# Kernel optimization log

Hardware: AMD Instinct MI355X
Metric: run time of the kernel (lower is better)

Reference implementation:

```python
import jax, jax.numpy as jnp
import numpy as np

B, T, D = 2, 4096, 1024
HQ, HKV, HD = 16, 4, 64   # 16 query heads, 4 KV heads (kv_groups=4), head_dim=64
WIN = 256                 # sliding window radius (left == right == 256)


def setup_inputs() -> dict:
    key = jax.random.key(0)
    ks = jax.random.split(key, 9)
    s = 0.02  # small init scale for stable softmax logits
    return {
        "x": jax.random.normal(ks[0], (B, T, D), jnp.float32),
        "wq": jax.random.normal(ks[1], (D, HQ * HD), jnp.float32) * s,
        "bq": jnp.zeros((HQ * HD,), jnp.float32),
        "wk": jax.random.normal(ks[2], (D, HKV * HD), jnp.float32) * s,
        "bk": jnp.zeros((HKV * HD,), jnp.float32),
        "wv": jax.random.normal(ks[3], (D, HKV * HD), jnp.float32) * s,
        "bv": jnp.zeros((HKV * HD,), jnp.float32),
        "wo": jax.random.normal(ks[4], (HQ * HD, D), jnp.float32) * s,
        "bo": jnp.zeros((D,), jnp.float32),
    }


def _banded_gqa(q, k, v, left, right):
    """Sliding-window GQA attention: query i attends keys in [i-left, i+right].
    Never materializes the full [B,H,T,T] score matrix; uses banded blocks."""
    Bq, Tq, Hq, d = q.shape
    Hkv = k.shape[2]
    G = Hq // Hkv                      # query heads per KV head
    bs = max(left, right)              # block size == window radius; T % bs == 0
    nb = Tq // bs
    # queries: [B, nb, bs, Hkv, G, d]
    qb = q.reshape(Bq, nb, bs, Hkv, G, d)
    # gather 3 neighboring key/value blocks per query block (pad one block each side)
    pad = ((0, 0), (bs, bs), (0, 0), (0, 0))
    idx = jnp.arange(nb)[:, None] * bs + jnp.arange(3 * bs)[None, :]  # into padded seq
    kctx = jnp.pad(k, pad)[:, idx]     # [B, nb, 3bs, Hkv, d]
    vctx = jnp.pad(v, pad)[:, idx]     # [B, nb, 3bs, Hkv, d]
    scale = 1.0 / jnp.sqrt(jnp.asarray(d, q.dtype))
    # banded scores: [B, nb, Hkv, G, bs, 3bs]
    scores = jnp.einsum('bnqhgd,bnkhd->bnhgqk', qb, kctx) * scale
    qpos = jnp.arange(nb)[:, None, None] * bs + jnp.arange(bs)[None, :, None]
    kpos = (jnp.arange(nb)[:, None, None] - 1) * bs + jnp.arange(3 * bs)[None, None, :]
    valid = (kpos >= 0) & (kpos < Tq) & (kpos >= qpos - left) & (kpos <= qpos + right)
    scores = jnp.where(valid[None, :, None, None, :, :], scores, jnp.asarray(-1e30, scores.dtype))
    p = jax.nn.softmax(scores, axis=-1)
    out = jnp.einsum('bnhgqk,bnkhd->bnqhgd', p, vctx)
    return out.reshape(Bq, Tq, Hq, d)


def reference(x, wq, bq, wk, bk, wv, bv, wo, bo):
    q = (x @ wq + bq).reshape(B, T, HQ, HD)
    k = (x @ wk + bk).reshape(B, T, HKV, HD)
    v = (x @ wv + bv).reshape(B, T, HKV, HD)
    y = _banded_gqa(q, k, v, WIN, WIN)       # [B, T, HQ, HD]
    y = y.reshape(B, T, HQ * HD)
    return y @ wo + bo                        # dropout=0.0, deterministic -> identity
```

## Files before the change

kernel.cpp:

```cpp
#include <hip/hip_runtime.h>

typedef unsigned short u16;
typedef u16 u16x4 __attribute__((ext_vector_type(4)));
typedef u16 u16x8 __attribute__((ext_vector_type(8)));
typedef __bf16 bf16x8 __attribute__((ext_vector_type(8)));
typedef float f32x4 __attribute__((ext_vector_type(4)));

#define DEVINL static __device__ __forceinline__

DEVINL u16 f2bf(float f) {
    unsigned u = __builtin_bit_cast(unsigned, f);
    u += 0x7fff + ((u >> 16) & 1);
    return (u16)(u >> 16);
}

DEVINL u16 pbf(float f) {
    unsigned u = __builtin_bit_cast(unsigned, f);
    return (u16)((u + 0x8000) >> 16);
}

DEVINL f32x4 mfma_bf16(u16x8 a, u16x8 b, f32x4 c) {
    return __builtin_amdgcn_mfma_f32_16x16x32_bf16(
        __builtin_bit_cast(bf16x8, a), __builtin_bit_cast(bf16x8, b), c, 0, 0, 0);
}

DEVINL void gload16(const void* g, void* lds) {
    __builtin_amdgcn_global_load_lds(
        (const __attribute__((address_space(1))) void*)g,
        (__attribute__((address_space(3))) void*)lds, 16, 0, 0);
}


__global__ void cvt_x_kernel(const float4* __restrict__ x4, u16x4* __restrict__ o4) {
    int idx = blockIdx.x * 256 + threadIdx.x;
    float4 a = x4[idx];
    u16x4 o;
    o[0] = f2bf(a.x); o[1] = f2bf(a.y); o[2] = f2bf(a.z); o[3] = f2bf(a.w);
    o4[idx] = o;
}

__global__ void fill_bias(const float* __restrict__ bq, const float* __restrict__ bk,
                          const float* __restrict__ bv, float* __restrict__ dst) {
    int i = blockIdx.x * 256 + threadIdx.x;
    if (i < 1024) dst[i] = bq[i];
    else if (i < 1280) dst[i] = bk[i - 1024];
    else if (i < 1536) dst[i] = bv[i - 1280];
}

__global__ void twt_kernel(const float* __restrict__ src, u16* __restrict__ dst,
                           int N, int rowOff) {
    __shared__ float t[64][65];
    int k0 = blockIdx.x * 64, n0 = blockIdx.y * 64;
    int tid = threadIdx.x;
#pragma unroll
    for (int j = 0; j < 16; j++) {
        int idx = j * 256 + tid; int r = idx >> 6, c = idx & 63;
        t[r][c] = src[(size_t)(k0 + r) * N + n0 + c];
    }
    __syncthreads();
#pragma unroll
    for (int j = 0; j < 16; j++) {
        int idx = j * 256 + tid; int r = idx >> 6, c = idx & 63;
        dst[(size_t)(rowOff + n0 + r) * 1024 + k0 + c] = f2bf(t[c][r]);
    }
}

__global__ void tv_kernel(const u16* __restrict__ qkv, u16* __restrict__ vt) {
    __shared__ u16 t[64][68];
    int t0 = blockIdx.x * 64; int h = blockIdx.y; int b = blockIdx.z;
    int tid = threadIdx.x;
#pragma unroll
    for (int j = 0; j < 16; j++) {
        int idx = j * 256 + tid; int r = idx >> 6, c = idx & 63;
        t[r][c] = qkv[(size_t)(b * 4096 + t0 + r) * 1536 + 1280 + h * 64 + c];
    }
    __syncthreads();
#pragma unroll
    for (int j = 0; j < 16; j++) {
        int idx = j * 256 + tid; int r = idx >> 6, c = idx & 63;
        vt[(size_t)((b * 4 + h) * 64 + r) * 4096 + t0 + c] = t[c][r];
    }
}


template <bool F32OUT>
__global__ __launch_bounds__(256, 2) void gemm_bt(
    const u16* __restrict__ A, const u16* __restrict__ Bt, void* __restrict__ Cp,
    const float* __restrict__ bias, int M, int N, int K, int qn, float qscale) {
    __shared__ __align__(16) u16 As[128 * 64];
    __shared__ __align__(16) u16 Bs[128 * 64];
    int tid = threadIdx.x; int l = tid & 63; int w = tid >> 6;

    int nwg = gridDim.x * gridDim.y;
    int lin = blockIdx.y * gridDim.x + blockIdx.x;
    int q_ = nwg >> 3, r_ = nwg & 7;
    int xcd = lin & 7, i_ = lin >> 3;
    int wgid = (xcd < r_ ? xcd * (q_ + 1) : r_ * (q_ + 1) + (xcd - r_) * q_) + i_;
    int m0 = (wgid / gridDim.x) * 128, n0 = (wgid % gridDim.x) * 128;

    int wm = (w >> 1) * 64, wn = (w & 1) * 64;
    f32x4 acc[4][4] = {};

    int srow[4], scol[4];
#pragma unroll
    for (int c = 0; c < 4; c++) {
        int b = (w * 4 + c) * 1024 + l * 16;
        int row = b >> 7, inner = b & 127;
        srow[c] = row;
        scol[c] = (inner ^ ((row & 7) << 4)) >> 1;
    }
    int nk = K >> 6;
    for (int kt = 0; kt < nk; ++kt) {
        int kb = kt << 6;
#pragma unroll
        for (int c = 0; c < 4; c++) {
            gload16(A + (size_t)(m0 + srow[c]) * K + kb + scol[c], (char*)As + (w * 4 + c) * 1024);
            gload16(Bt + (size_t)(n0 + srow[c]) * K + kb + scol[c], (char*)Bs + (w * 4 + c) * 1024);
        }
        __syncthreads();
#pragma unroll
        for (int kc = 0; kc < 2; ++kc) {
            int co = (kc * 32 + (l >> 4) * 8) * 2;
            u16x8 af[4], bf[4];
#pragma unroll
            for (int mf = 0; mf < 4; ++mf) {
                int row = wm + mf * 16 + (l & 15);
                af[mf] = *(const u16x8*)((const char*)As + row * 128 + (co ^ ((row & 7) << 4)));
            }
#pragma unroll
            for (int nf = 0; nf < 4; ++nf) {
                int row = wn + nf * 16 + (l & 15);
                bf[nf] = *(const u16x8*)((const char*)Bs + row * 128 + (co ^ ((row & 7) << 4)));
            }
#pragma unroll
            for (int mf = 0; mf < 4; ++mf)
#pragma unroll
                for (int nf = 0; nf < 4; ++nf)
                    acc[mf][nf] = mfma_bf16(af[mf], bf[nf], acc[mf][nf]);
        }
        __syncthreads();
    }
#pragma unroll
    for (int mf = 0; mf < 4; ++mf) {
#pragma unroll
        for (int nf = 0; nf < 4; ++nf) {
            int col = n0 + wn + nf * 16 + (l & 15);
            float bv = bias ? bias[col] : 0.0f;
            float scl = (col < qn) ? qscale : 1.0f;
#pragma unroll
            for (int r = 0; r < 4; r++) {
                int row = m0 + wm + mf * 16 + (l >> 4) * 4 + r;
                float v = (acc[mf][nf][r] + bv) * scl;
                if (F32OUT) ((float*)Cp)[(size_t)row * N + col] = v;
                else        ((u16*)Cp)[(size_t)row * N + col] = f2bf(v);
            }
        }
    }
}


__global__ __launch_bounds__(512, 4) void attn_kernel(
    const u16* __restrict__ qkv, const u16* __restrict__ vt, u16* __restrict__ y) {
    __shared__ __align__(16) u16 Ks[64 * 64];
    __shared__ __align__(16) u16 Vs[64 * 64];
    __shared__ __align__(16) u16 Ps[8][16 * 64];
    int tid = threadIdx.x, l = tid & 63, w = tid >> 6;
    int qb = ((blockIdx.x & 7) << 3) | (blockIdx.x >> 3);
    int h = blockIdx.y >> 1, hp = blockIdx.y & 1, b = blockIdx.z;
    int qstart = qb * 64;
    size_t rowbase = (size_t)b * 4096;
    int hq = h * 4 + hp * 2 + (w >> 2);
    int qrow0 = (w & 3) * 16;

    u16x8 qf_[2];
#pragma unroll
    for (int kc = 0; kc < 2; ++kc)
        qf_[kc] = *(const u16x8*)(qkv + (rowbase + qstart + qrow0 + (l & 15)) * 1536
                                  + hq * 64 + kc * 32 + (l >> 4) * 8);

    f32x4 o[4] = {};
    float mrow = -__builtin_inff(), srow_ = 0.f;

    const u16* kbase_ptr = qkv + 1024 + h * 64;
    const u16* vbase_ptr = vt + (size_t)((b * 4 + h) * 64) * 4096;

    int sb_ = w * 1024 + l * 16;
    int g_row = sb_ >> 7, g_inner = sb_ & 127;
    int g_col = (g_inner ^ ((g_row & 7) << 4)) >> 1;

#pragma unroll
    for (int kstart = qstart - 256; kstart <= qstart + 256; kstart += 64) {
        if (kstart < 0 || kstart >= 4096) continue;
        gload16(kbase_ptr + (rowbase + kstart + g_row) * 1536 + g_col, (char*)Ks + w * 1024);
        gload16(vbase_ptr + (size_t)g_row * 4096 + kstart + g_col, (char*)Vs + w * 1024);
        __syncthreads();

        f32x4 st[4] = {};
#pragma unroll
        for (int kc = 0; kc < 2; ++kc) {
            int co = (kc * 32 + (l >> 4) * 8) * 2;
#pragma unroll
            for (int kf = 0; kf < 4; ++kf) {
                int row = kf * 16 + (l & 15);
                u16x8 kfr = *(const u16x8*)((const char*)Ks + row * 128 + (co ^ ((row & 7) << 4)));
                st[kf] = mfma_bf16(kfr, qf_[kc], st[kf]);
            }
        }

        bool mlo = (kstart == qstart - 256);
        bool mhi = (kstart == qstart + 256);

        int qoff = qrow0 + (l & 15);
        float pmax = -1e30f;
        float sv[4][4];
#pragma unroll
        for (int kf = 0; kf < 4; ++kf)
#pragma unroll
            for (int r = 0; r < 4; r++) {
                int koff = kf * 16 + (l >> 4) * 4 + r;
                float v = st[kf][r];
                if (mlo && koff < qoff) v = -1e30f;
                if (mhi && koff > qoff) v = -1e30f;
                sv[kf][r] = v;
                pmax = fmaxf(pmax, v);
            }
        pmax = fmaxf(pmax, __shfl_xor(pmax, 16));
        pmax = fmaxf(pmax, __shfl_xor(pmax, 32));

        bool resc = !__all(pmax - mrow <= 8.0f);
        float newm = resc ? fmaxf(mrow, pmax) : mrow;
        float psum = 0.f;
#pragma unroll
        for (int kf = 0; kf < 4; ++kf) {
            u16x4 pk;
#pragma unroll
            for (int r = 0; r < 4; r++) {
                float e = __builtin_amdgcn_exp2f(sv[kf][r] - newm);
                psum += e;
                pk[r] = pbf(e);
            }
            int row = l & 15;
            int keyc = kf * 16 + (l >> 4) * 4;
            *(u16x4*)((char*)Ps[w] + ((row * 128 + keyc * 2) ^ ((row & 7) << 4))) = pk;
        }
        psum += __shfl_xor(psum, 16);
        psum += __shfl_xor(psum, 32);
        if (resc) {
            float fs = __builtin_amdgcn_exp2f(mrow - newm);
            srow_ = srow_ * fs + psum;
            mrow = newm;
#pragma unroll
            for (int r = 0; r < 4; r++) {
                float fb = __shfl(fs, (l >> 4) * 4 + r);
#pragma unroll
                for (int nf = 0; nf < 4; ++nf) o[nf][r] *= fb;
            }
        } else {
            srow_ += psum;
        }

#pragma unroll
        for (int kc = 0; kc < 2; ++kc) {
            int co = (kc * 32 + (l >> 4) * 8) * 2;
            int prow = l & 15;
            u16x8 pa = *(const u16x8*)((const char*)Ps[w] + ((prow * 128 + co) ^ ((prow & 7) << 4)));
#pragma unroll
            for (int nf = 0; nf < 4; ++nf) {
                int row = nf * 16 + (l & 15);
                u16x8 vb = *(const u16x8*)((const char*)Vs + row * 128 + (co ^ ((row & 7) << 4)));
                o[nf] = mfma_bf16(pa, vb, o[nf]);
            }
        }
        __syncthreads();
    }

    float inv = 1.0f / srow_;
#pragma unroll
    for (int r = 0; r < 4; r++) {
        float sb = __shfl(inv, (l >> 4) * 4 + r);
        int row = qstart + qrow0 + (l >> 4) * 4 + r;
#pragma unroll
        for (int nf = 0; nf < 4; ++nf) {
            int col = hq * 64 + nf * 16 + (l & 15);
            y[(rowbase + row) * 1024 + col] = f2bf(o[nf][r] * sb);
        }
    }
}


extern "C" void kernel_launch(void* const* d_in, const int* in_sizes, int n_in,
                              void* d_out, int out_size, void* d_ws, size_t ws_size,
                              hipStream_t stream) {
    const float* x  = (const float*)d_in[0];
    const float* wq = (const float*)d_in[1];
    const float* bq = (const float*)d_in[2];
    const float* wk = (const float*)d_in[3];
    const float* bk = (const float*)d_in[4];
    const float* wv = (const float*)d_in[5];
    const float* bv = (const float*)d_in[6];
    const float* wo = (const float*)d_in[7];
    const float* bo = (const float*)d_in[8];
    float* out = (float*)d_out;

    char* p = (char*)d_ws;
    u16* xb     = (u16*)p;   p += (size_t)8192 * 1024 * 2;
    u16* wqkvt  = (u16*)p;   p += (size_t)1536 * 1024 * 2;
    u16* wot    = (u16*)p;   p += (size_t)1024 * 1024 * 2;
    float* bqkv = (float*)p; p += 8192;
    u16* qkvb   = (u16*)p;   p += (size_t)8192 * 1536 * 2;
    u16* vtb    = (u16*)p;   p += (size_t)512 * 4096 * 2;
    u16* yb     = (u16*)p;

    cvt_x_kernel<<<8192, 256, 0, stream>>>((const float4*)x, (u16x4*)xb);
    fill_bias<<<6, 256, 0, stream>>>(bq, bk, bv, bqkv);
    twt_kernel<<<dim3(16, 16), 256, 0, stream>>>(wq, wqkvt, 1024, 0);
    twt_kernel<<<dim3(16, 4),  256, 0, stream>>>(wk, wqkvt, 256, 1024);
    twt_kernel<<<dim3(16, 4),  256, 0, stream>>>(wv, wqkvt, 256, 1280);
    twt_kernel<<<dim3(16, 16), 256, 0, stream>>>(wo, wot, 1024, 0);

    gemm_bt<false><<<dim3(12, 64), 256, 0, stream>>>(xb, wqkvt, qkvb, bqkv,
                                                     8192, 1536, 1024, 1024, 0.18033688f);
    tv_kernel<<<dim3(64, 4, 2), 256, 0, stream>>>(qkvb, vtb);
    attn_kernel<<<dim3(64, 8, 2), 512, 0, stream>>>(qkvb, vtb, yb);
    gemm_bt<true><<<dim3(8, 64), 256, 0, stream>>>(yb, wot, out, bo,
                                                   8192, 1024, 1024, 0, 1.0f);
}
```

Before: 118.8 us.

## Split attention blocks to one query head per 256-thread block

The attention kernel now assigns a single query head per block (4 waves, 256 threads) instead of two heads across 8 waves, doubling the grid along the head dimension and shrinking the P scratch buffer. Each thread now loads two 16-byte K/V chunks per tile to fill shared memory with half the threads. The max and sum reductions are also restructured into tree form to shorten dependency chains. The trade-off is that K/V tiles are loaded from global memory twice as often, because the two heads in a pair no longer share a tile, in exchange for smaller blocks and potentially higher occupancy.

```diff
diff --git a/kernel.cpp b/kernel.cpp
--- a/kernel.cpp
+++ b/kernel.cpp
@@ -159,18 +159,18 @@
 }
 
 
-__global__ __launch_bounds__(512, 4) void attn_kernel(
+__global__ __launch_bounds__(256, 6) void attn_kernel(
     const u16* __restrict__ qkv, const u16* __restrict__ vt, u16* __restrict__ y) {
     __shared__ __align__(16) u16 Ks[64 * 64];
     __shared__ __align__(16) u16 Vs[64 * 64];
-    __shared__ __align__(16) u16 Ps[8][16 * 64];
+    __shared__ __align__(16) u16 Ps[4][16 * 64];
     int tid = threadIdx.x, l = tid & 63, w = tid >> 6;
     int qb = ((blockIdx.x & 7) << 3) | (blockIdx.x >> 3);
-    int h = blockIdx.y >> 1, hp = blockIdx.y & 1, b = blockIdx.z;
+    int hq = blockIdx.y, b = blockIdx.z;
+    int h = hq >> 2;
     int qstart = qb * 64;
     size_t rowbase = (size_t)b * 4096;
-    int hq = h * 4 + hp * 2 + (w >> 2);
-    int qrow0 = (w & 3) * 16;
+    int qrow0 = w * 16;
 
     u16x8 qf_[2];
 #pragma unroll
@@ -184,15 +184,25 @@
     const u16* kbase_ptr = qkv + 1024 + h * 64;
     const u16* vbase_ptr = vt + (size_t)((b * 4 + h) * 64) * 4096;
 
-    int sb_ = w * 1024 + l * 16;
-    int g_row = sb_ >> 7, g_inner = sb_ & 127;
-    int g_col = (g_inner ^ ((g_row & 7) << 4)) >> 1;
+    int g_row[2], g_col[2];
+#pragma unroll
+    for (int c = 0; c < 2; c++) {
+        int sb_ = (w * 2 + c) * 1024 + l * 16;
+        int row = sb_ >> 7, inner = sb_ & 127;
+        g_row[c] = row;
+        g_col[c] = (inner ^ ((row & 7) << 4)) >> 1;
+    }
 
 #pragma unroll
     for (int kstart = qstart - 256; kstart <= qstart + 256; kstart += 64) {
         if (kstart < 0 || kstart >= 4096) continue;
-        gload16(kbase_ptr + (rowbase + kstart + g_row) * 1536 + g_col, (char*)Ks + w * 1024);
-        gload16(vbase_ptr + (size_t)g_row * 4096 + kstart + g_col, (char*)Vs + w * 1024);
+#pragma unroll
+        for (int c = 0; c < 2; c++) {
+            gload16(kbase_ptr + (rowbase + kstart + g_row[c]) * 1536 + g_col[c],
+                    (char*)Ks + (w * 2 + c) * 1024);
+            gload16(vbase_ptr + (size_t)g_row[c] * 4096 + kstart + g_col[c],
+                    (char*)Vs + (w * 2 + c) * 1024);
+        }
         __syncthreads();
 
         f32x4 st[4] = {};
@@ -211,10 +221,10 @@
         bool mhi = (kstart == qstart + 256);
 
         int qoff = qrow0 + (l & 15);
-        float pmax = -1e30f;
         float sv[4][4];
-#pragma unroll
-        for (int kf = 0; kf < 4; ++kf)
+        float kmax[4];
+#pragma unroll
+        for (int kf = 0; kf < 4; ++kf) {
 #pragma unroll
             for (int r = 0; r < 4; r++) {
                 int koff = kf * 16 + (l >> 4) * 4 + r;
@@ -222,27 +232,30 @@
                 if (mlo && koff < qoff) v = -1e30f;
                 if (mhi && koff > qoff) v = -1e30f;
                 sv[kf][r] = v;
-                pmax = fmaxf(pmax, v);
-            }
+            }
+            kmax[kf] = fmaxf(fmaxf(sv[kf][0], sv[kf][1]), fmaxf(sv[kf][2], sv[kf][3]));
+        }
+        float pmax = fmaxf(fmaxf(kmax[0], kmax[1]), fmaxf(kmax[2], kmax[3]));
         pmax = fmaxf(pmax, __shfl_xor(pmax, 16));
         pmax = fmaxf(pmax, __shfl_xor(pmax, 32));
 
         bool resc = !__all(pmax - mrow <= 8.0f);
         float newm = resc ? fmaxf(mrow, pmax) : mrow;
-        float psum = 0.f;
+        float ps[4];
 #pragma unroll
         for (int kf = 0; kf < 4; ++kf) {
+            float e0 = __builtin_amdgcn_exp2f(sv[kf][0] - newm);
+            float e1 = __builtin_amdgcn_exp2f(sv[kf][1] - newm);
+            float e2 = __builtin_amdgcn_exp2f(sv[kf][2] - newm);
+            float e3 = __builtin_amdgcn_exp2f(sv[kf][3] - newm);
+            ps[kf] = (e0 + e1) + (e2 + e3);
             u16x4 pk;
-#pragma unroll
-            for (int r = 0; r < 4; r++) {
-                float e = __builtin_amdgcn_exp2f(sv[kf][r] - newm);
-                psum += e;
-                pk[r] = pbf(e);
-            }
+            pk[0] = pbf(e0); pk[1] = pbf(e1); pk[2] = pbf(e2); pk[3] = pbf(e3);
             int row = l & 15;
             int keyc = kf * 16 + (l >> 4) * 4;
             *(u16x4*)((char*)Ps[w] + ((row * 128 + keyc * 2) ^ ((row & 7) << 4))) = pk;
         }
+        float psum = (ps[0] + ps[1]) + (ps[2] + ps[3]);
         psum += __shfl_xor(psum, 16);
         psum += __shfl_xor(psum, 32);
         if (resc) {
@@ -321,7 +334,7 @@
     gemm_bt<false><<<dim3(12, 64), 256, 0, stream>>>(xb, wqkvt, qkvb, bqkv,
                                                      8192, 1536, 1024, 1024, 0.18033688f);
     tv_kernel<<<dim3(64, 4, 2), 256, 0, stream>>>(qkvb, vtb);
-    attn_kernel<<<dim3(64, 8, 2), 512, 0, stream>>>(qkvb, vtb, yb);
+    attn_kernel<<<dim3(64, 16, 2), 256, 0, stream>>>(qkvb, vtb, yb);
     gemm_bt<true><<<dim3(8, 64), 256, 0, stream>>>(yb, wot, out, bo,
                                                    8192, 1024, 1024, 0, 1.0f);
 }
```

New measurement: 126.3 us. 6.3% more time.

## Replace 128x128 GEMM with double-buffered 256x256 tile pipelined kernel

Applied to the files above, without the earlier changes.

Replaces the 128x128-tile, 256-thread GEMM with a 256x256-tile, 512-thread kernel. It double-buffers A and B in LDS and staggers the next tiles' global-to-LDS loads across four MFMA sub-steps, using explicit waitcnt, barrier and setprio control. The aim is to hide global load latency behind MFMA work and get more reuse per LDS load. In exchange the grids shrink to 192 and 128 workgroups, fewer than the CU count, with 128KB of LDS per block. At the end of the K loop the prefetch wraps around and loads tiles that are never used.

```diff
diff --git a/kernel.cpp b/kernel.cpp
--- a/kernel.cpp
+++ b/kernel.cpp
@@ -84,72 +84,113 @@
 
 
 template <bool F32OUT>
-__global__ __launch_bounds__(256, 2) void gemm_bt(
+__global__ __launch_bounds__(512, 2) void gemm256(
     const u16* __restrict__ A, const u16* __restrict__ Bt, void* __restrict__ Cp,
     const float* __restrict__ bias, int M, int N, int K, int qn, float qscale) {
-    __shared__ __align__(16) u16 As[128 * 64];
-    __shared__ __align__(16) u16 Bs[128 * 64];
-    int tid = threadIdx.x; int l = tid & 63; int w = tid >> 6;
+    __shared__ __align__(16) u16 lds[2][2][2][8192];
+    int tid = threadIdx.x, l = tid & 63, w = tid >> 6;
+    int wr = w >> 2, wc = w & 3;
 
     int nwg = gridDim.x * gridDim.y;
     int lin = blockIdx.y * gridDim.x + blockIdx.x;
     int q_ = nwg >> 3, r_ = nwg & 7;
     int xcd = lin & 7, i_ = lin >> 3;
     int wgid = (xcd < r_ ? xcd * (q_ + 1) : r_ * (q_ + 1) + (xcd - r_) * q_) + i_;
-    int m0 = (wgid / gridDim.x) * 128, n0 = (wgid % gridDim.x) * 128;
-
-    int wm = (w >> 1) * 64, wn = (w & 1) * 64;
-    f32x4 acc[4][4] = {};
-
-    int srow[4], scol[4];
-#pragma unroll
-    for (int c = 0; c < 4; c++) {
-        int b = (w * 4 + c) * 1024 + l * 16;
-        int row = b >> 7, inner = b & 127;
-        srow[c] = row;
-        scol[c] = (inner ^ ((row & 7) << 4)) >> 1;
-    }
-    int nk = K >> 6;
-    for (int kt = 0; kt < nk; ++kt) {
-        int kb = kt << 6;
-#pragma unroll
-        for (int c = 0; c < 4; c++) {
-            gload16(A + (size_t)(m0 + srow[c]) * K + kb + scol[c], (char*)As + (w * 4 + c) * 1024);
-            gload16(Bt + (size_t)(n0 + srow[c]) * K + kb + scol[c], (char*)Bs + (w * 4 + c) * 1024);
-        }
-        __syncthreads();
-#pragma unroll
-        for (int kc = 0; kc < 2; ++kc) {
-            int co = (kc * 32 + (l >> 4) * 8) * 2;
-            u16x8 af[4], bf[4];
-#pragma unroll
-            for (int mf = 0; mf < 4; ++mf) {
-                int row = wm + mf * 16 + (l & 15);
-                af[mf] = *(const u16x8*)((const char*)As + row * 128 + (co ^ ((row & 7) << 4)));
-            }
-#pragma unroll
-            for (int nf = 0; nf < 4; ++nf) {
-                int row = wn + nf * 16 + (l & 15);
-                bf[nf] = *(const u16x8*)((const char*)Bs + row * 128 + (co ^ ((row & 7) << 4)));
-            }
-#pragma unroll
-            for (int mf = 0; mf < 4; ++mf)
+    int m0 = (wgid / gridDim.x) * 256, n0 = (wgid % gridDim.x) * 256;
+
+    f32x4 acc[8][4] = {};
+
+    int srow_[2], scol_[2];
+#pragma unroll
+    for (int c = 0; c < 2; c++) {
+        int off = (w * 2 + c) * 1024 + l * 16;
+        int row = off >> 7, inner = off & 127;
+        srow_[c] = row;
+        scol_[c] = (inner ^ ((row & 7) << 4)) >> 1;
+    }
+
+#define STG(dp, ab, h, base, kb)                                                    \
+    do {                                                                            \
+        _Pragma("unroll")                                                           \
+        for (int c = 0; c < 2; c++)                                                 \
+            gload16((base) + (size_t)((h) * 128 + srow_[c]) * K + (kb) + scol_[c],  \
+                    (char*)&lds[dp][ab][h][0] + (w * 2 + c) * 1024);                \
+    } while (0)
+
+    const u16* Ab = A + (size_t)m0 * K;
+    const u16* Bb = Bt + (size_t)n0 * K;
+    int NKT = K >> 6, mask = NKT - 1;
+
+    STG(0, 0, 0, Ab, 0); STG(0, 0, 1, Ab, 0);
+    STG(0, 1, 0, Bb, 0); STG(0, 1, 1, Bb, 0);
+    STG(1, 1, 0, Bb, 64); STG(1, 1, 1, Bb, 64);
+    asm volatile("s_waitcnt vmcnt(0)" ::: "memory");
+    __builtin_amdgcn_s_barrier();
+
+    for (int T = 0; T < NKT; ++T) {
+        int p = T & 1;
+        int kbA = ((T + 1) & mask) << 6;
+        int kbB = ((T + 2) & mask) << 6;
+        u16x8 bfr[4][2];
+#pragma unroll
+        for (int s = 0; s < 4; ++s) {
+            u16x8 afr[2][2];
+#pragma unroll
+            for (int mi = 0; mi < 2; ++mi)
+#pragma unroll
+                for (int kc = 0; kc < 2; ++kc) {
+                    int row = (2 * s + mi) * 16 + (l & 15);
+                    int co = (kc * 32 + (l >> 4) * 8) * 2;
+                    afr[mi][kc] = *(const u16x8*)((const char*)&lds[p][0][wr][0]
+                                  + row * 128 + (co ^ ((row & 7) << 4)));
+                }
+            if (s == 0) {
 #pragma unroll
                 for (int nf = 0; nf < 4; ++nf)
-                    acc[mf][nf] = mfma_bf16(af[mf], bf[nf], acc[mf][nf]);
-        }
-        __syncthreads();
-    }
-#pragma unroll
-    for (int mf = 0; mf < 4; ++mf) {
+#pragma unroll
+                    for (int kc = 0; kc < 2; ++kc) {
+                        int row = (wc & 1) * 64 + nf * 16 + (l & 15);
+                        int co = (kc * 32 + (l >> 4) * 8) * 2;
+                        bfr[nf][kc] = *(const u16x8*)((const char*)&lds[p][1][wc >> 1][0]
+                                      + row * 128 + (co ^ ((row & 7) << 4)));
+                    }
+            }
+            if (s == 0)      STG(p ^ 1, 0, 0, Ab, kbA);
+            else if (s == 1) STG(p ^ 1, 0, 1, Ab, kbA);
+            else if (s == 2) STG(p, 1, 0, Bb, kbB);
+            else {
+                STG(p, 1, 1, Bb, kbB);
+                asm volatile("s_waitcnt vmcnt(4)" ::: "memory");
+            }
+            __builtin_amdgcn_s_barrier();
+            asm volatile("s_waitcnt lgkmcnt(0)" ::: "memory");
+            __builtin_amdgcn_sched_barrier(0);
+            __builtin_amdgcn_s_setprio(1);
+#pragma unroll
+            for (int kc = 0; kc < 2; ++kc)
+#pragma unroll
+                for (int mi = 0; mi < 2; ++mi)
+#pragma unroll
+                    for (int nf = 0; nf < 4; ++nf)
+                        acc[2 * s + mi][nf] =
+                            mfma_bf16(afr[mi][kc], bfr[nf][kc], acc[2 * s + mi][nf]);
+            __builtin_amdgcn_s_setprio(0);
+            __builtin_amdgcn_s_barrier();
+        }
+    }
+#undef STG
+    asm volatile("s_waitcnt vmcnt(0)" ::: "memory");
+
+#pragma unroll
+    for (int mf = 0; mf < 8; ++mf) {
 #pragma unroll
         for (int nf = 0; nf < 4; ++nf) {
-            int col = n0 + wn + nf * 16 + (l & 15);
+            int col = n0 + wc * 64 + nf * 16 + (l & 15);
             float bv = bias ? bias[col] : 0.0f;
             float scl = (col < qn) ? qscale : 1.0f;
 #pragma unroll
             for (int r = 0; r < 4; r++) {
-                int row = m0 + wm + mf * 16 + (l >> 4) * 4 + r;
+                int row = m0 + wr * 128 + mf * 16 + (l >> 4) * 4 + r;
                 float v = (acc[mf][nf][r] + bv) * scl;
                 if (F32OUT) ((float*)Cp)[(size_t)row * N + col] = v;
                 else        ((u16*)Cp)[(size_t)row * N + col] = f2bf(v);
@@ -318,10 +359,10 @@
     twt_kernel<<<dim3(16, 4),  256, 0, stream>>>(wv, wqkvt, 256, 1280);
     twt_kernel<<<dim3(16, 16), 256, 0, stream>>>(wo, wot, 1024, 0);
 
-    gemm_bt<false><<<dim3(12, 64), 256, 0, stream>>>(xb, wqkvt, qkvb, bqkv,
-                                                     8192, 1536, 1024, 1024, 0.18033688f);
+    gemm256<false><<<dim3(6, 32), 512, 0, stream>>>(xb, wqkvt, qkvb, bqkv,
+                                                    8192, 1536, 1024, 1024, 0.18033688f);
     tv_kernel<<<dim3(64, 4, 2), 256, 0, stream>>>(qkvb, vtb);
     attn_kernel<<<dim3(64, 8, 2), 512, 0, stream>>>(qkvb, vtb, yb);
-    gemm_bt<true><<<dim3(8, 64), 256, 0, stream>>>(yb, wot, out, bo,
+    gemm256<true><<<dim3(4, 32), 512, 0, stream>>>(yb, wot, out, bo,
                                                    8192, 1024, 1024, 0, 1.0f);
 }
```

Result: slower. 136.3 us (+14.7%).
